# Kernel optimization log

Measured on AMD Instinct MI355X. Metric: run time of the kernel, lower is better.

The kernel has to match this reference:

```python
import jax, jax.numpy as jnp
import numpy as np

TEMPERATURE = 0.07
LOG_EPS = 1e-20
MEAN_EPS = 1e-6


def setup_inputs() -> dict:
    key = jax.random.key(0)
    k1, k2, k3 = jax.random.split(key, 3)
    B, T1, I1, C = 64, 33, 197, 512  # 1+seqlen=33, 1+14*14=197
    text_embeds = jax.random.normal(k1, (B, T1, C), dtype=jnp.float32)
    video_embeds = jax.random.normal(k2, (B, I1, C), dtype=jnp.float32)
    text_attn_mask = jax.random.randint(k3, (B, T1), 0, 2).astype(jnp.int32)
    # guarantee every row has at least one attended (non-CLS) token
    text_attn_mask = text_attn_mask.at[:, :2].set(1)
    return {"text_embeds": text_embeds, "video_embeds": video_embeds,
            "text_attn_mask": text_attn_mask}


def reference(text_embeds, video_embeds, text_attn_mask):
    # NOTE: original normalizes over dim=1 (sequence axis), kept faithfully.
    te = text_embeds / jnp.linalg.norm(text_embeds, axis=1, keepdims=True)
    ve = video_embeds / jnp.linalg.norm(video_embeds, axis=1, keepdims=True)
    mask = text_attn_mask[:, 1:].astype(bool)          # [B, T] (trim CLS)
    text_latents = te[:, 1:, :]                        # [B, T, C]
    # full late-interaction score tensor, scaled (multiplied) by temperature
    sim = jnp.einsum('xtd,yid->xyti', text_latents, ve) * TEMPERATURE  # [X,Y,T,I]

    # text -> image: max over image tokens, masked mean over text tokens
    t2i = sim.max(axis=-1)                             # [X, Y, T]
    m = mask[None, :, None, :]                         # [1, B, 1, T] (X must == B)
    numer = jnp.where(m, t2i[None], 0.0).sum(axis=-1)  # [1, B, Y]
    denom = jnp.maximum(mask.sum(axis=-1).astype(sim.dtype), MEAN_EPS)[None, :, None]
    text_to_image = numer / denom                      # [1, B, Y]

    # image -> text: masked max over text tokens, mean over image tokens
    # (computed in the original module but unused in the returned loss)
    m5 = mask[None, :, None, :, None]                  # [1, B, 1, T, 1]
    neg = -jnp.finfo(sim.dtype).max
    image_to_text = jnp.where(m5, sim[None], neg).max(axis=-2).mean(axis=-1)  # [1,B,Y]
    del image_to_text  # dead in original: loss = text_to_image_loss only

    t2i_exp = jnp.exp(text_to_image)                   # [1, B, Y]
    pos = jnp.diagonal(t2i_exp, axis1=-2, axis2=-1)    # [1, min(B, Y)]
    den = t2i_exp.sum(axis=-1)                         # [1, B]
    loss = -jnp.log(pos / den + LOG_EPS).mean(axis=-1)  # [1]
    return loss
```

## Files before the change

kernel.cpp:

```cpp
#include <hip/hip_runtime.h>
#include <hip/hip_bf16.h>
#include <float.h>
#include <math.h>

#define BB 64
#define T1 33
#define TT 32
#define II 197
#define CC 512
#define TEMP 0.07f

typedef float f32x4 __attribute__((ext_vector_type(4)));
typedef int i32x4 __attribute__((ext_vector_type(4)));
typedef int i32x8 __attribute__((ext_vector_type(8)));

#define TL_OFF  0
#define VE_OFF  (1 << 20)
#define TTI_OFF ((1 << 20) + (8 << 20))
#define KS_STRIDE   32768
#define GRP_STRIDE  131072

__global__ __launch_bounds__(256) void norm_all_kernel(const float* __restrict__ text,
                                                       const float* __restrict__ video,
                                                       unsigned char* __restrict__ tl8,
                                                       unsigned char* __restrict__ ve8) {
  int b = blockIdx.x, hz = blockIdx.y, tid = threadIdx.x;
  bool isV = hz < 4;
  int h2 = isV ? hz : hz - 4;
  const float* src = isV ? (video + (size_t)b * II * CC) : (text + (size_t)b * T1 * CC);
  int n = isV ? II : T1;

  __shared__ float red[8][128];
  __shared__ float rn[128];

  {
    int c4 = tid & 31, rg = tid >> 5;
    const float* p = src + h2 * 128 + c4 * 4;
    float4 s = {0.f, 0.f, 0.f, 0.f};
    for (int i = rg; i < n; i += 8) {
      float4 v = *(const float4*)(p + (size_t)i * CC);
      s.x += v.x * v.x; s.y += v.y * v.y; s.z += v.z * v.z; s.w += v.w * v.w;
    }
    *(float4*)&red[rg][c4 * 4] = s;
  }
  __syncthreads();
  if (tid < 128) {
    float s = 0.f;
#pragma unroll
    for (int g = 0; g < 8; ++g) s += red[g][tid];
    rn[tid] = 1.0f / sqrtf(s);
  }
  __syncthreads();

  if (isV) {
    for (int S = tid; S < 13 * 128; S += 256) {
      int fb = S >> 7, h = (S >> 6) & 1, lane = S & 63;
      int i = fb * 16 + (lane & 15);
      int kloc = ((lane >> 4) & 3) * 32 + h * 16;
      float4 u[4] = {};
      if (i < II) {
        const float* p = src + (size_t)i * CC + h2 * 128 + kloc;
#pragma unroll
        for (int q = 0; q < 4; ++q) u[q] = *(const float4*)(p + q * 4);
      }
      unsigned int wd[4];
#pragma unroll
      for (int q = 0; q < 4; ++q) {
        float4 r = *(const float4*)&rn[kloc + q * 4];
        int wv = __builtin_amdgcn_cvt_pk_fp8_f32(u[q].x * r.x, u[q].y * r.y, 0, 0);
        wv = __builtin_amdgcn_cvt_pk_fp8_f32(u[q].z * r.z, u[q].w * r.w, wv, 1);
        wd[q] = (unsigned int)wv;
      }
      unsigned char* dst = ve8 + (size_t)b * GRP_STRIDE + h2 * KS_STRIDE +
                           fb * 2048 + h * 1024 + lane * 16;
      *(uint4*)dst = make_uint4(wd[0], wd[1], wd[2], wd[3]);
    }
  } else {
    int fa_local = tid >> 7, h = (tid >> 6) & 1, lane = tid & 63;
    int t = fa_local * 16 + (lane & 15);
    int kloc = ((lane >> 4) & 3) * 32 + h * 16;
    const float* p = src + (size_t)(1 + t) * CC + h2 * 128 + kloc;
    unsigned int wd[4];
#pragma unroll
    for (int q = 0; q < 4; ++q) {
      float4 u = *(const float4*)(p + q * 4);
      float4 r = *(const float4*)&rn[kloc + q * 4];
      int wv = __builtin_amdgcn_cvt_pk_fp8_f32(u.x * r.x, u.y * r.y, 0, 0);
      wv = __builtin_amdgcn_cvt_pk_fp8_f32(u.z * r.z, u.w * r.w, wv, 1);
      wd[q] = (unsigned int)wv;
    }
    int fa = (b & 7) * 2 + fa_local;
    unsigned char* dst = tl8 + (size_t)(b >> 3) * GRP_STRIDE + h2 * KS_STRIDE +
                         fa * 2048 + h * 1024 + lane * 16;
    *(uint4*)dst = make_uint4(wd[0], wd[1], wd[2], wd[3]);
  }
}

typedef __attribute__((address_space(3))) unsigned int lds_u32;
typedef __attribute__((address_space(1))) const unsigned int glb_u32;
__device__ __forceinline__ void gl16(const unsigned char* g, unsigned char* l) {
  __builtin_amdgcn_global_load_lds((glb_u32*)(const void*)g, (lds_u32*)(void*)l, 16, 0, 0);
}

__global__ __launch_bounds__(512, 2) void sim_kernel(const unsigned char* __restrict__ tl8,
                                                     const unsigned char* __restrict__ ve8,
                                                     const int* __restrict__ mask,
                                                     float* __restrict__ tti) {
  int L = blockIdx.x;
  int xcd = L & 7;
  int idx = L >> 3;
  int y = xcd * 8 + (idx & 7);
  int xcb = idx >> 3;

  int tid = threadIdx.x;
  int w = tid >> 6, lane = tid & 63;
  int wm = w >> 2;
  int wn = w & 3;

  __shared__ __attribute__((aligned(16))) unsigned char As[3][8 * 2048];
  __shared__ __attribute__((aligned(16))) unsigned char Bs[3][16 * 2048];
  __shared__ float smax[4 * 128];

  const unsigned char* Abase =
      tl8 + (size_t)(xcb >> 1) * GRP_STRIDE + (size_t)(xcb & 1) * 8 * 2048;
  const unsigned char* Bbase = ve8 + (size_t)y * GRP_STRIDE;

#define STG(s_) do {                                                          \
    int slot_ = (s_) % 3;                                                     \
    _Pragma("unroll")                                                         \
    for (int r_ = 0; r_ < 6; ++r_) {                                          \
      int g_ = w * 6 + r_;                                                    \
      if (g_ < 16) {                                                          \
        int fa_ = g_ >> 1, h_ = g_ & 1;                                       \
        const unsigned char* src_ =                                           \
            Abase + (size_t)(s_) * KS_STRIDE + fa_ * 2048 + h_ * 1024 + lane * 16; \
        gl16(src_, &As[slot_][(fa_ * 2 + h_) * 1024 + lane * 16]);            \
      } else {                                                                \
        int gb_ = g_ - 16;                                                    \
        int fb_ = gb_ >> 1, h_ = gb_ & 1;                                     \
        const unsigned char* src_ =                                           \
            Bbase + (size_t)(s_) * KS_STRIDE + fb_ * 2048 + h_ * 1024 + lane * 16; \
        gl16(src_, &Bs[slot_][(fb_ * 2 + h_) * 1024 + lane * 16]);            \
      }                                                                       \
    }                                                                         \
  } while (0)

#define KCOMPUTE(slot_, NF_) do {                                             \
    i32x8 aop_[4];                                                            \
    _Pragma("unroll")                                                         \
    for (int ma_ = 0; ma_ < 4; ++ma_) {                                       \
      i32x4 h0_ = *(const i32x4*)&As[slot_][((wm * 4 + ma_) * 2) * 1024 + lane * 16]; \
      i32x4 h1_ = *(const i32x4*)&As[slot_][((wm * 4 + ma_) * 2 + 1) * 1024 + lane * 16]; \
      aop_[ma_] = __builtin_shufflevector(h0_, h1_, 0, 1, 2, 3, 4, 5, 6, 7);  \
    }                                                                         \
    i32x8 bop_[NF_];                                                          \
    _Pragma("unroll")                                                         \
    for (int nb_ = 0; nb_ < NF_; ++nb_) {                                     \
      int fb_ = wn + 4 * nb_;                                                 \
      i32x4 h0_ = *(const i32x4*)&Bs[slot_][(fb_ * 2) * 1024 + lane * 16];    \
      i32x4 h1_ = *(const i32x4*)&Bs[slot_][(fb_ * 2 + 1) * 1024 + lane * 16]; \
      bop_[nb_] = __builtin_shufflevector(h0_, h1_, 0, 1, 2, 3, 4, 5, 6, 7);  \
    }                                                                         \
    __builtin_amdgcn_s_setprio(1);                                            \
    _Pragma("unroll")                                                         \
    for (int ma_ = 0; ma_ < 4; ++ma_)                                         \
      _Pragma("unroll")                                                       \
      for (int nb_ = 0; nb_ < NF_; ++nb_)                                     \
        acc[ma_][nb_] = __builtin_amdgcn_mfma_scale_f32_16x16x128_f8f6f4(     \
            aop_[ma_], bop_[nb_], acc[ma_][nb_], 0, 0,                        \
            0, 0x7F7F7F7F, 0, 0x7F7F7F7F);                                    \
    __builtin_amdgcn_s_setprio(0);                                            \
  } while (0)

  f32x4 acc[4][4] = {};

  STG(0); STG(1);
  asm volatile("s_waitcnt vmcnt(6)" ::: "memory");
  __builtin_amdgcn_s_barrier();

  STG(2);
  if (wn == 0) KCOMPUTE(0, 4); else KCOMPUTE(0, 3);
  asm volatile("s_waitcnt vmcnt(6)" ::: "memory");
  __builtin_amdgcn_s_barrier();
  STG(3);
  if (wn == 0) KCOMPUTE(1, 4); else KCOMPUTE(1, 3);
  asm volatile("s_waitcnt vmcnt(6)" ::: "memory");
  __builtin_amdgcn_s_barrier();
  if (wn == 0) KCOMPUTE(2, 4); else KCOMPUTE(2, 3);
  asm volatile("s_waitcnt vmcnt(0)" ::: "memory");
  __builtin_amdgcn_s_barrier();
  if (wn == 0) KCOMPUTE(0, 4); else KCOMPUTE(0, 3);
#undef STG
#undef KCOMPUTE

  int col = lane & 15, gq = lane >> 4;
  int nfrag = (wn == 0) ? 4 : 3;
  bool valid[4];
#pragma unroll
  for (int nb = 0; nb < 4; ++nb) {
    int fb = wn + 4 * nb;
    valid[nb] = (nb < nfrag) && (fb * 16 + col < II);
  }

  float mx[4][4];
#pragma unroll
  for (int ma = 0; ma < 4; ++ma)
#pragma unroll
    for (int reg = 0; reg < 4; ++reg) {
      float m = -FLT_MAX;
#pragma unroll
      for (int nb = 0; nb < 4; ++nb)
        if (valid[nb]) m = fmaxf(m, acc[ma][nb][reg]);
      mx[ma][reg] = m;
    }
#pragma unroll
  for (int st = 1; st <= 8; st <<= 1)
#pragma unroll
    for (int ma = 0; ma < 4; ++ma)
#pragma unroll
      for (int reg = 0; reg < 4; ++reg)
        mx[ma][reg] = fmaxf(mx[ma][reg], __shfl_xor(mx[ma][reg], st));

  if (col == 0) {
#pragma unroll
    for (int ma = 0; ma < 4; ++ma)
#pragma unroll
      for (int reg = 0; reg < 4; ++reg)
        smax[wn * 128 + wm * 64 + ma * 16 + gq * 4 + reg] = mx[ma][reg];
  }
  __syncthreads();

  if (tid < 128) {
    int r = tid;
    float m = fmaxf(fmaxf(smax[r], smax[128 + r]),
                    fmaxf(smax[256 + r], smax[384 + r]));
    int x = xcb * 4 + (r >> 5), tt = r & 31;
    int mk = mask[x * T1 + 1 + tt];
    float num = mk ? m * TEMP : 0.f;
    float cnt = mk ? 1.f : 0.f;
#pragma unroll
    for (int st = 1; st < 32; st <<= 1) {
      num += __shfl_xor(num, st);
      cnt += __shfl_xor(cnt, st);
    }
    if (tt == 0) tti[x * 64 + y] = num / fmaxf(cnt, 1e-6f);
  }
}

__global__ void loss_kernel(const float* __restrict__ tti, float* __restrict__ out) {
  __shared__ float lxs[64];
  int tid = threadIdx.x;
  int x = tid >> 4, q = tid & 15;
  float4 v = *(const float4*)&tti[x * 64 + q * 4];
  float den = expf(v.x) + expf(v.y) + expf(v.z) + expf(v.w);
#pragma unroll
  for (int st = 1; st < 16; st <<= 1) den += __shfl_xor(den, st);
  if (q == 0) {
    float pos = expf(tti[x * 64 + x]);
    lxs[x] = -logf(pos / den + 1e-20f);
  }
  __syncthreads();
  if (tid < 64) {
    float lx = lxs[tid];
#pragma unroll
    for (int s = 1; s < 64; s <<= 1) lx += __shfl_xor(lx, s);
    if (tid == 0) out[0] = lx * (1.0f / 64.0f);
  }
}

extern "C" void kernel_launch(void* const* d_in, const int* in_sizes, int n_in,
                              void* d_out, int out_size, void* d_ws, size_t ws_size,
                              hipStream_t stream) {
  const float* text = (const float*)d_in[0];
  const float* video = (const float*)d_in[1];
  const int* mask = (const int*)d_in[2];
  float* out = (float*)d_out;

  char* ws = (char*)d_ws;
  unsigned char* tl8 = (unsigned char*)(ws + TL_OFF);
  unsigned char* ve8 = (unsigned char*)(ws + VE_OFF);
  float* tti = (float*)(ws + TTI_OFF);

  hipLaunchKernelGGL(norm_all_kernel, dim3(BB, 8), dim3(256), 0, stream, text, video, tl8, ve8);
  hipLaunchKernelGGL(sim_kernel, dim3(1024), dim3(512), 0, stream, tl8, ve8, mask, tti);
  hipLaunchKernelGGL(loss_kernel, dim3(1), dim3(1024), 0, stream, tti, out);
}
```

Measured before the change: 50.61 us.

## Cache normalized rows in LDS and shrink sim kernel LDS for higher occupancy

The norm kernel now runs 512 threads per block and stores each fp32 tile in shared memory during the norm pass, so the fp8 conversion pass reads from LDS instead of reading global memory a second time. The sim kernel moves from a triple-buffered to a double-buffered LDS pipeline. It keeps only 12 of the 13 B fragments in LDS and has the wn==0 waves load the last fragment straight into registers. smax aliases As, which needs an extra barrier, and launch bounds are raised to allow 4 blocks per CU. The trade-off is less prefetch depth and more register pressure, plus a ~104KB LDS cache in the norm kernel that limits that kernel's occupancy.

```diff
diff --git a/kernel.cpp b/kernel.cpp
--- a/kernel.cpp
+++ b/kernel.cpp
@@ -20,7 +20,7 @@
 #define KS_STRIDE   32768
 #define GRP_STRIDE  131072
 
-__global__ __launch_bounds__(256) void norm_all_kernel(const float* __restrict__ text,
+__global__ __launch_bounds__(512) void norm_all_kernel(const float* __restrict__ text,
                                                        const float* __restrict__ video,
                                                        unsigned char* __restrict__ tl8,
                                                        unsigned char* __restrict__ ve8) {
@@ -30,15 +30,17 @@
   const float* src = isV ? (video + (size_t)b * II * CC) : (text + (size_t)b * T1 * CC);
   int n = isV ? II : T1;
 
-  __shared__ float red[8][128];
+  __shared__ float cache[II][132];
+  __shared__ float red[16][128];
   __shared__ float rn[128];
 
   {
     int c4 = tid & 31, rg = tid >> 5;
     const float* p = src + h2 * 128 + c4 * 4;
     float4 s = {0.f, 0.f, 0.f, 0.f};
-    for (int i = rg; i < n; i += 8) {
+    for (int i = rg; i < n; i += 16) {
       float4 v = *(const float4*)(p + (size_t)i * CC);
+      *(float4*)&cache[i][c4 * 4] = v;
       s.x += v.x * v.x; s.y += v.y * v.y; s.z += v.z * v.z; s.w += v.w * v.w;
     }
     *(float4*)&red[rg][c4 * 4] = s;
@@ -47,46 +49,41 @@
   if (tid < 128) {
     float s = 0.f;
 #pragma unroll
-    for (int g = 0; g < 8; ++g) s += red[g][tid];
+    for (int g = 0; g < 16; ++g) s += red[g][tid];
     rn[tid] = 1.0f / sqrtf(s);
   }
   __syncthreads();
 
   if (isV) {
-    for (int S = tid; S < 13 * 128; S += 256) {
+    for (int S = tid; S < 13 * 128; S += 512) {
       int fb = S >> 7, h = (S >> 6) & 1, lane = S & 63;
       int i = fb * 16 + (lane & 15);
       int kloc = ((lane >> 4) & 3) * 32 + h * 16;
-      float4 u[4] = {};
-      if (i < II) {
-        const float* p = src + (size_t)i * CC + h2 * 128 + kloc;
-#pragma unroll
-        for (int q = 0; q < 4; ++q) u[q] = *(const float4*)(p + q * 4);
-      }
       unsigned int wd[4];
 #pragma unroll
       for (int q = 0; q < 4; ++q) {
-        float4 r = *(const float4*)&rn[kloc + q * 4];
-        int wv = __builtin_amdgcn_cvt_pk_fp8_f32(u[q].x * r.x, u[q].y * r.y, 0, 0);
-        wv = __builtin_amdgcn_cvt_pk_fp8_f32(u[q].z * r.z, u[q].w * r.w, wv, 1);
+        f32x4 u = {0.f, 0.f, 0.f, 0.f};
+        if (i < II) u = *(const f32x4*)&cache[i][kloc + q * 4];
+        f32x4 r = *(const f32x4*)&rn[kloc + q * 4];
+        int wv = __builtin_amdgcn_cvt_pk_fp8_f32(u[0] * r[0], u[1] * r[1], 0, 0);
+        wv = __builtin_amdgcn_cvt_pk_fp8_f32(u[2] * r[2], u[3] * r[3], wv, 1);
         wd[q] = (unsigned int)wv;
       }
       unsigned char* dst = ve8 + (size_t)b * GRP_STRIDE + h2 * KS_STRIDE +
                            fb * 2048 + h * 1024 + lane * 16;
       *(uint4*)dst = make_uint4(wd[0], wd[1], wd[2], wd[3]);
     }
-  } else {
+  } else if (tid < 256) {
     int fa_local = tid >> 7, h = (tid >> 6) & 1, lane = tid & 63;
     int t = fa_local * 16 + (lane & 15);
     int kloc = ((lane >> 4) & 3) * 32 + h * 16;
-    const float* p = src + (size_t)(1 + t) * CC + h2 * 128 + kloc;
     unsigned int wd[4];
 #pragma unroll
     for (int q = 0; q < 4; ++q) {
-      float4 u = *(const float4*)(p + q * 4);
-      float4 r = *(const float4*)&rn[kloc + q * 4];
-      int wv = __builtin_amdgcn_cvt_pk_fp8_f32(u.x * r.x, u.y * r.y, 0, 0);
-      wv = __builtin_amdgcn_cvt_pk_fp8_f32(u.z * r.z, u.w * r.w, wv, 1);
+      f32x4 u = *(const f32x4*)&cache[1 + t][kloc + q * 4];
+      f32x4 r = *(const f32x4*)&rn[kloc + q * 4];
+      int wv = __builtin_amdgcn_cvt_pk_fp8_f32(u[0] * r[0], u[1] * r[1], 0, 0);
+      wv = __builtin_amdgcn_cvt_pk_fp8_f32(u[2] * r[2], u[3] * r[3], wv, 1);
       wd[q] = (unsigned int)wv;
     }
     int fa = (b & 7) * 2 + fa_local;
@@ -102,7 +99,7 @@
   __builtin_amdgcn_global_load_lds((glb_u32*)(const void*)g, (lds_u32*)(void*)l, 16, 0, 0);
 }
 
-__global__ __launch_bounds__(512, 2) void sim_kernel(const unsigned char* __restrict__ tl8,
+__global__ __launch_bounds__(512, 4) void sim_kernel(const unsigned char* __restrict__ tl8,
                                                      const unsigned char* __restrict__ ve8,
                                                      const int* __restrict__ mask,
                                                      float* __restrict__ tti) {
@@ -117,19 +114,19 @@
   int wm = w >> 2;
   int wn = w & 3;
 
-  __shared__ __attribute__((aligned(16))) unsigned char As[3][8 * 2048];
-  __shared__ __attribute__((aligned(16))) unsigned char Bs[3][16 * 2048];
-  __shared__ float smax[4 * 128];
+  __shared__ __attribute__((aligned(16))) unsigned char As[2][8 * 2048];
+  __shared__ __attribute__((aligned(16))) unsigned char Bs[2][12 * 2048];
+  float* smax = (float*)&As[0][0];
 
   const unsigned char* Abase =
       tl8 + (size_t)(xcb >> 1) * GRP_STRIDE + (size_t)(xcb & 1) * 8 * 2048;
   const unsigned char* Bbase = ve8 + (size_t)y * GRP_STRIDE;
 
 #define STG(s_) do {                                                          \
-    int slot_ = (s_) % 3;                                                     \
-    _Pragma("unroll")                                                         \
-    for (int r_ = 0; r_ < 6; ++r_) {                                          \
-      int g_ = w * 6 + r_;                                                    \
+    int slot_ = (s_) & 1;                                                     \
+    _Pragma("unroll")                                                         \
+    for (int r_ = 0; r_ < 5; ++r_) {                                          \
+      int g_ = w * 5 + r_;                                                    \
       if (g_ < 16) {                                                          \
         int fa_ = g_ >> 1, h_ = g_ & 1;                                       \
         const unsigned char* src_ =                                           \
@@ -145,7 +142,13 @@
     }                                                                         \
   } while (0)
 
-#define KCOMPUTE(slot_, NF_) do {                                             \
+#define LD12(s_, dst_) do {                                                   \
+    const unsigned char* p_ = Bbase + (size_t)(s_) * KS_STRIDE + 12 * 2048 + lane * 16; \
+    dst_##h0 = *(const i32x4*)(p_);                                           \
+    dst_##h1 = *(const i32x4*)(p_ + 1024);                                    \
+  } while (0)
+
+#define KCOMPUTE(slot_, F12_) do {                                            \
     i32x8 aop_[4];                                                            \
     _Pragma("unroll")                                                         \
     for (int ma_ = 0; ma_ < 4; ++ma_) {                                       \
@@ -153,44 +156,93 @@
       i32x4 h1_ = *(const i32x4*)&As[slot_][((wm * 4 + ma_) * 2 + 1) * 1024 + lane * 16]; \
       aop_[ma_] = __builtin_shufflevector(h0_, h1_, 0, 1, 2, 3, 4, 5, 6, 7);  \
     }                                                                         \
-    i32x8 bop_[NF_];                                                          \
-    _Pragma("unroll")                                                         \
-    for (int nb_ = 0; nb_ < NF_; ++nb_) {                                     \
+    int nf_ = (F12_) ? 4 : 3;                                                 \
+    i32x8 bop_[4];                                                            \
+    _Pragma("unroll")                                                         \
+    for (int nb_ = 0; nb_ < 3; ++nb_) {                                       \
       int fb_ = wn + 4 * nb_;                                                 \
       i32x4 h0_ = *(const i32x4*)&Bs[slot_][(fb_ * 2) * 1024 + lane * 16];    \
       i32x4 h1_ = *(const i32x4*)&Bs[slot_][(fb_ * 2 + 1) * 1024 + lane * 16]; \
       bop_[nb_] = __builtin_shufflevector(h0_, h1_, 0, 1, 2, 3, 4, 5, 6, 7);  \
     }                                                                         \
+    if ((F12_) == 1) bop_[3] = __builtin_shufflevector(frAh0, frAh1, 0, 1, 2, 3, 4, 5, 6, 7); \
+    if ((F12_) == 2) bop_[3] = __builtin_shufflevector(frBh0, frBh1, 0, 1, 2, 3, 4, 5, 6, 7); \
     __builtin_amdgcn_s_setprio(1);                                            \
     _Pragma("unroll")                                                         \
     for (int ma_ = 0; ma_ < 4; ++ma_)                                         \
       _Pragma("unroll")                                                       \
-      for (int nb_ = 0; nb_ < NF_; ++nb_)                                     \
-        acc[ma_][nb_] = __builtin_amdgcn_mfma_scale_f32_16x16x128_f8f6f4(     \
-            aop_[ma_], bop_[nb_], acc[ma_][nb_], 0, 0,                        \
-            0, 0x7F7F7F7F, 0, 0x7F7F7F7F);                                    \
+      for (int nb_ = 0; nb_ < 4; ++nb_)                                       \
+        if (nb_ < nf_)                                                        \
+          acc[ma_][nb_] = __builtin_amdgcn_mfma_scale_f32_16x16x128_f8f6f4(   \
+              aop_[ma_], bop_[nb_], acc[ma_][nb_], 0, 0,                      \
+              0, 0x7F7F7F7F, 0, 0x7F7F7F7F);                                  \
     __builtin_amdgcn_s_setprio(0);                                            \
   } while (0)
 
   f32x4 acc[4][4] = {};
-
-  STG(0); STG(1);
-  asm volatile("s_waitcnt vmcnt(6)" ::: "memory");
-  __builtin_amdgcn_s_barrier();
-
-  STG(2);
-  if (wn == 0) KCOMPUTE(0, 4); else KCOMPUTE(0, 3);
-  asm volatile("s_waitcnt vmcnt(6)" ::: "memory");
-  __builtin_amdgcn_s_barrier();
-  STG(3);
-  if (wn == 0) KCOMPUTE(1, 4); else KCOMPUTE(1, 3);
-  asm volatile("s_waitcnt vmcnt(6)" ::: "memory");
-  __builtin_amdgcn_s_barrier();
-  if (wn == 0) KCOMPUTE(2, 4); else KCOMPUTE(2, 3);
+  i32x4 frAh0, frAh1, frBh0, frBh1;
+
+  STG(0);
+  if (wn == 0) LD12(0, frA);
   asm volatile("s_waitcnt vmcnt(0)" ::: "memory");
   __builtin_amdgcn_s_barrier();
-  if (wn == 0) KCOMPUTE(0, 4); else KCOMPUTE(0, 3);
+
+  STG(1);
+  if (wn == 0) {
+    LD12(1, frB);
+    KCOMPUTE(0, 1);
+    asm volatile("s_waitcnt vmcnt(2)" ::: "memory");
+  } else {
+    KCOMPUTE(0, 0);
+    asm volatile("s_waitcnt vmcnt(0)" ::: "memory");
+  }
+  __builtin_amdgcn_s_barrier();
+
+  STG(0 + 2 - 2);
 #undef STG
+#define STG2(s_, slot_) do {                                                  \
+    _Pragma("unroll")                                                         \
+    for (int r_ = 0; r_ < 5; ++r_) {                                          \
+      int g_ = w * 5 + r_;                                                    \
+      if (g_ < 16) {                                                          \
+        int fa_ = g_ >> 1, h_ = g_ & 1;                                       \
+        const unsigned char* src_ =                                           \
+            Abase + (size_t)(s_) * KS_STRIDE + fa_ * 2048 + h_ * 1024 + lane * 16; \
+        gl16(src_, &As[slot_][(fa_ * 2 + h_) * 1024 + lane * 16]);            \
+      } else {                                                                \
+        int gb_ = g_ - 16;                                                    \
+        int fb_ = gb_ >> 1, h_ = gb_ & 1;                                     \
+        const unsigned char* src_ =                                           \
+            Bbase + (size_t)(s_) * KS_STRIDE + fb_ * 2048 + h_ * 1024 + lane * 16; \
+        gl16(src_, &Bs[slot_][(fb_ * 2 + h_) * 1024 + lane * 16]);            \
+      }                                                                       \
+    }                                                                         \
+  } while (0)
+  if (wn == 0) {
+    LD12(2, frA);
+    KCOMPUTE(1, 2);
+    asm volatile("s_waitcnt vmcnt(2)" ::: "memory");
+  } else {
+    KCOMPUTE(1, 0);
+    asm volatile("s_waitcnt vmcnt(0)" ::: "memory");
+  }
+  __builtin_amdgcn_s_barrier();
+
+  STG2(3, 1);
+  if (wn == 0) {
+    LD12(3, frB);
+    KCOMPUTE(0, 1);
+    asm volatile("s_waitcnt vmcnt(2)" ::: "memory");
+  } else {
+    KCOMPUTE(0, 0);
+    asm volatile("s_waitcnt vmcnt(0)" ::: "memory");
+  }
+  __builtin_amdgcn_s_barrier();
+
+  if (wn == 0) KCOMPUTE(1, 2);
+  else         KCOMPUTE(1, 0);
+#undef STG2
+#undef LD12
 #undef KCOMPUTE
 
   int col = lane & 15, gq = lane >> 4;
@@ -221,6 +273,7 @@
       for (int reg = 0; reg < 4; ++reg)
         mx[ma][reg] = fmaxf(mx[ma][reg], __shfl_xor(mx[ma][reg], st));
 
+  __syncthreads();
   if (col == 0) {
 #pragma unroll
     for (int ma = 0; ma < 4; ++ma)
@@ -281,7 +334,7 @@
   unsigned char* ve8 = (unsigned char*)(ws + VE_OFF);
   float* tti = (float*)(ws + TTI_OFF);
 
-  hipLaunchKernelGGL(norm_all_kernel, dim3(BB, 8), dim3(256), 0, stream, text, video, tl8, ve8);
+  hipLaunchKernelGGL(norm_all_kernel, dim3(BB, 8), dim3(512), 0, stream, text, video, tl8, ve8);
   hipLaunchKernelGGL(sim_kernel, dim3(1024), dim3(512), 0, stream, tl8, ve8, mask, tti);
   hipLaunchKernelGGL(loss_kernel, dim3(1), dim3(1024), 0, stream, tti, out);
 }
```

Measured after the change: 92.66 us. 1.83x slower.
